# Performance work log

Measured on AMD Instinct MI355X. Metric: run time of the kernel, lower is better.

The kernel has to match this reference:

```python
import jax, jax.numpy as jnp
import numpy as np

B, T, C, H = 4, 2048, 1024, 16
INIT_STD = 0.02

def setup_inputs() -> dict:
    key = jax.random.key(0)
    ks = jax.random.split(key, 9)
    x = jax.random.normal(ks[0], (B, T, C), dtype=jnp.float32)
    def dense(kw):
        return jax.random.normal(kw, (C, C), dtype=jnp.float32) * INIT_STD
    return {
        "x": x,
        "Wq": dense(ks[1]), "bq": jnp.zeros((C,), jnp.float32),
        "Wk": dense(ks[2]), "bk": jnp.zeros((C,), jnp.float32),
        "Wv": dense(ks[3]), "bv": jnp.zeros((C,), jnp.float32),
        "Wo": dense(ks[4]), "bo": jnp.zeros((C,), jnp.float32),
    }

def reference(x, Wq, bq, Wk, bk, Wv, bv, Wo, bo):
    b, t, c = x.shape
    hd = c // H  # head dim
    # QKV projections, reshape to (B, H, T, hd)
    def split_heads(y):
        return jnp.transpose(y.reshape(b, t, H, hd), (0, 2, 1, 3))
    q = split_heads(x @ Wq + bq)
    k = split_heads(x @ Wk + bk)
    v = split_heads(x @ Wv + bv)
    scale = 1.0 / jnp.sqrt(jnp.float32(hd))
    att = jnp.einsum('bhqd,bhkd->bhqk', q, k) * scale  # [B,H,T,T]
    mask = jnp.tril(jnp.ones((t, t), dtype=bool))[None, None]
    att = jnp.where(mask, att, jnp.float32(-jnp.inf))
    att = jax.nn.softmax(att, axis=-1)
    y = jnp.einsum('bhqk,bhkd->bhqd', att, v)  # [B,H,T,hd]
    y = jnp.transpose(y, (0, 2, 1, 3)).reshape(b, t, c)
    return y @ Wo + bo
```

## Files before the change

kernel.cpp:

```cpp
#include <hip/hip_runtime.h>
#include <hip/hip_bf16.h>
#include <stdint.h>

typedef __bf16 bf16;
typedef __attribute__((ext_vector_type(8))) __bf16 bf16x8;
typedef __attribute__((ext_vector_type(4))) __bf16 bf16x4;
typedef __attribute__((ext_vector_type(4))) float f32x4;

constexpr int Bn = 4, Tn = 2048, Cn = 1024, Hn = 16, HD = 64;
constexpr int Mn = Bn * Tn;

__device__ __forceinline__ void gl_lds16(const void* g, void* l) {
  __builtin_amdgcn_global_load_lds(
      (const __attribute__((address_space(1))) void*)g,
      (__attribute__((address_space(3))) void*)l, 16u, 0, 0u);
}

__global__ __launch_bounds__(256) void k_cvt_x(const float* __restrict__ x,
                                               bf16* __restrict__ xb) {
  int i = (blockIdx.x * 256 + threadIdx.x) * 8;
  float4 a = *(const float4*)(x + i);
  float4 b = *(const float4*)(x + i + 4);
  bf16x8 v;
  v[0] = (bf16)a.x; v[1] = (bf16)a.y; v[2] = (bf16)a.z; v[3] = (bf16)a.w;
  v[4] = (bf16)b.x; v[5] = (bf16)b.y; v[6] = (bf16)b.z; v[7] = (bf16)b.w;
  *(bf16x8*)(xb + i) = v;
}

__global__ __launch_bounds__(256) void k_tw(const float* __restrict__ W0,
                                            const float* __restrict__ W1,
                                            const float* __restrict__ W2,
                                            const float* __restrict__ W3,
                                            bf16* __restrict__ WT) {
  __shared__ float tile[32][33];
  const float* W = (blockIdx.z == 0) ? W0 : (blockIdx.z == 1) ? W1
                  : (blockIdx.z == 2) ? W2 : W3;
  bf16* out = WT + (size_t)blockIdx.z * Cn * Cn;
  int tx = threadIdx.x & 31, ty = threadIdx.x >> 5;
  int gx = blockIdx.x * 32 + tx;
  int gy = blockIdx.y * 32;
#pragma unroll
  for (int j = 0; j < 32; j += 8)
    tile[ty + j][tx] = W[(size_t)(gy + ty + j) * Cn + gx];
  __syncthreads();
  int ox = blockIdx.y * 32 + tx;
  int oy = blockIdx.x * 32;
#pragma unroll
  for (int j = 0; j < 32; j += 8)
    out[(size_t)(oy + ty + j) * Cn + ox] = (bf16)tile[tx][ty + j];
}

__global__ __launch_bounds__(256) void k_gemm_qkv(const bf16* __restrict__ A,
                                                  const bf16* __restrict__ BT,
                                                  const float* __restrict__ bq,
                                                  const float* __restrict__ bk,
                                                  const float* __restrict__ bv,
                                                  bf16* __restrict__ out,
                                                  float qscale) {
  constexpr int KD = 1024;
  __shared__ __align__(16) bf16 As[128 * 64];
  __shared__ __align__(16) bf16 Bs[128 * 64];
  const int t = threadIdx.x;
  const int w = t >> 6, l = t & 63;
  const int b = blockIdx.x;
  const int k8 = b & 7, j = b >> 3;
  const int m0 = (j / 3) * 128, n0 = (3 * k8 + j % 3) * 128;
  const int wr = (w >> 1) * 64, wc = (w & 1) * 64;
  f32x4 acc[4][4] = {};

  for (int kt = 0; kt < KD; kt += 64) {
    __syncthreads();
#pragma unroll
    for (int i = 0; i < 4; ++i) {
      int c = i * 256 + t;
      int row = c >> 3;
      int seg = (c & 7) ^ (row & 7);
      gl_lds16(A + (size_t)(m0 + row) * KD + kt + seg * 8,
               (char*)As + i * 4096 + w * 1024);
      gl_lds16(BT + (size_t)(n0 + row) * KD + kt + seg * 8,
               (char*)Bs + i * 4096 + w * 1024);
    }
    __syncthreads();
#pragma unroll
    for (int kc = 0; kc < 2; ++kc) {
      bf16x8 af[4], bg[4];
#pragma unroll
      for (int mi = 0; mi < 4; ++mi) {
        int row = wr + mi * 16 + (l & 15);
        int off = (row * 128 + kc * 64 + (l >> 4) * 16) ^ ((row & 7) << 4);
        af[mi] = *(const bf16x8*)((const char*)As + off);
      }
#pragma unroll
      for (int ni = 0; ni < 4; ++ni) {
        int row = wc + ni * 16 + (l & 15);
        int off = (row * 128 + kc * 64 + (l >> 4) * 16) ^ ((row & 7) << 4);
        bg[ni] = *(const bf16x8*)((const char*)Bs + off);
      }
#pragma unroll
      for (int mi = 0; mi < 4; ++mi)
#pragma unroll
        for (int ni = 0; ni < 4; ++ni)
          acc[mi][ni] = __builtin_amdgcn_mfma_f32_16x16x32_bf16(
              af[mi], bg[ni], acc[mi][ni], 0, 0, 0);
    }
  }
  const int q16l = l & 15;
#pragma unroll
  for (int ni = 0; ni < 4; ++ni) {
    int colBase = n0 + wc + ni * 16;
    int which = colBase >> 10;
    const float* bp = (which == 0) ? bq : (which == 1) ? bk : bv;
    float scl = (which == 0) ? qscale : 1.0f;
    float bval = bp[(colBase & 1023) + q16l];
    int hh = (colBase >> 6) & 15;
    int dd = (colBase & 63) + q16l;
    size_t obase = (size_t)which * 8388608 + (size_t)hh * (Tn * HD) + dd;
#pragma unroll
    for (int mi = 0; mi < 4; ++mi) {
#pragma unroll
      for (int r = 0; r < 4; ++r) {
        int row = m0 + wr + mi * 16 + (l >> 4) * 4 + r;
        int bb = row >> 11, tt = row & 2047;
        float v = (acc[mi][ni][r] + bval) * scl;
        out[obase + ((size_t)bb * Hn * Tn + tt) * HD] = (bf16)v;
      }
    }
  }
}

__global__ __launch_bounds__(256) void k_gemm_o(const bf16* __restrict__ A,
                                                const bf16* __restrict__ BT,
                                                const float* __restrict__ bias,
                                                float* __restrict__ out) {
  constexpr int KD = 1024;
  __shared__ __align__(16) bf16 As[128 * 64];
  __shared__ __align__(16) bf16 Bs[128 * 64];
  const int t = threadIdx.x;
  const int w = t >> 6, l = t & 63;
  const int b = blockIdx.x;
  const int m0 = (b >> 3) * 128, n0 = (b & 7) * 128;
  const int wr = (w >> 1) * 64, wc = (w & 1) * 64;
  f32x4 acc[4][4] = {};

  for (int kt = 0; kt < KD; kt += 64) {
    __syncthreads();
#pragma unroll
    for (int i = 0; i < 4; ++i) {
      int c = i * 256 + t;
      int row = c >> 3;
      int seg = (c & 7) ^ (row & 7);
      gl_lds16(A + (size_t)(m0 + row) * KD + kt + seg * 8,
               (char*)As + i * 4096 + w * 1024);
      gl_lds16(BT + (size_t)(n0 + row) * KD + kt + seg * 8,
               (char*)Bs + i * 4096 + w * 1024);
    }
    __syncthreads();
#pragma unroll
    for (int kc = 0; kc < 2; ++kc) {
      bf16x8 af[4], bg[4];
#pragma unroll
      for (int mi = 0; mi < 4; ++mi) {
        int row = wr + mi * 16 + (l & 15);
        int off = (row * 128 + kc * 64 + (l >> 4) * 16) ^ ((row & 7) << 4);
        af[mi] = *(const bf16x8*)((const char*)As + off);
      }
#pragma unroll
      for (int ni = 0; ni < 4; ++ni) {
        int row = wc + ni * 16 + (l & 15);
        int off = (row * 128 + kc * 64 + (l >> 4) * 16) ^ ((row & 7) << 4);
        bg[ni] = *(const bf16x8*)((const char*)Bs + off);
      }
#pragma unroll
      for (int mi = 0; mi < 4; ++mi)
#pragma unroll
        for (int ni = 0; ni < 4; ++ni)
          acc[mi][ni] = __builtin_amdgcn_mfma_f32_16x16x32_bf16(
              af[mi], bg[ni], acc[mi][ni], 0, 0, 0);
    }
  }
#pragma unroll
  for (int ni = 0; ni < 4; ++ni) {
    int col = n0 + wc + ni * 16 + (l & 15);
    float bv = bias[col];
#pragma unroll
    for (int mi = 0; mi < 4; ++mi) {
#pragma unroll
      for (int r = 0; r < 4; ++r) {
        int row = m0 + wr + mi * 16 + (l >> 4) * 4 + r;
        out[(size_t)row * Cn + col] = acc[mi][ni][r] + bv;
      }
    }
  }
}

__global__ __launch_bounds__(512, 4) void k_attn(const bf16* __restrict__ Q,
                                                 const bf16* __restrict__ K,
                                                 const bf16* __restrict__ V,
                                                 bf16* __restrict__ Y) {
  __shared__ __align__(16) char smem[32768];
  const int t = threadIdx.x, w = t >> 6, l = t & 63;
  const int g = l >> 4, q16 = l & 15;
  const int wg = blockIdx.x;
  const int bh = wg & 63;
  const int qtile = 15 - (wg >> 6);
  const size_t base = (size_t)bh * Tn * HD;
  const bf16* Qh = Q + base;
  const bf16* Vh = V + base;
  const int qg = qtile * 128 + w * 16 + q16;

  bf16x8 aq[2];
#pragma unroll
  for (int kc = 0; kc < 2; ++kc)
    aq[kc] = *(const bf16x8*)(Qh + (size_t)qg * HD + kc * 32 + g * 8);

  const int xm = (q16 & 7) << 4;
  const int qkB0 = q16 * 128 + ((g * 16) ^ xm);
  const int qkB1 = q16 * 128 + ((64 + g * 16) ^ xm);
  const int innerL = (l >> 5) * 64 + ((l & 15) >> 2) * 16 +
                     (((l >> 4) & 1) * 4 + (l & 3)) * 2;
  int stb[8];
#pragma unroll
  for (int j = 0; j < 8; ++j)
    stb[j] = w * 1024 + j * 128 + (innerL ^ (j << 4));

  const int krow = w * 8 + (l >> 3);
  const int kseg = (l & 7) ^ (krow & 7);
  const bf16* kP = K + base + (size_t)krow * HD + kseg * 8;
  const bf16* vP = Vh + (size_t)l * HD + w * 8;

  f32x4 yacc[4] = {};
  float m_ = -1e30f, l_ = 0.f;
  const int nt = 2 * qtile + 2;
  const int it_mask = 2 * qtile + (w >= 4 ? 1 : 0);
  const int diag = (w & 3) * 16 + q16;

#define STAGE_K(KBUF)                           \
  {                                             \
    gl_lds16(kP, smem + (KBUF) + w * 1024);     \
    kP += 4096;                                 \
  }
#define WRITE_V(VBUF, a0)                               \
  {                                                     \
    _Pragma("unroll") for (int j = 0; j < 8; ++j)       \
      *(bf16*)(smem + (VBUF) + stb[j]) = a0[j];         \
  }
#define COMPUTE(KBUF, VBUF, DOMASK)                                          \
  {                                                                          \
    f32x4 s[4] = {};                                                         \
    __builtin_amdgcn_s_setprio(1);                                           \
    _Pragma("unroll") for (int nj = 0; nj < 4; ++nj) {                       \
      bf16x8 ak0 = *(const bf16x8*)(smem + (KBUF) + qkB0 + nj * 2048);       \
      s[nj] = __builtin_amdgcn_mfma_f32_16x16x32_bf16(ak0, aq[0], s[nj], 0, 0, 0); \
      bf16x8 ak1 = *(const bf16x8*)(smem + (KBUF) + qkB1 + nj * 2048);       \
      s[nj] = __builtin_amdgcn_mfma_f32_16x16x32_bf16(ak1, aq[1], s[nj], 0, 0, 0); \
    }                                                                        \
    __builtin_amdgcn_s_setprio(0);                                           \
    if (DOMASK) {                                                            \
      _Pragma("unroll") for (int nj = 0; nj < 4; ++nj)                       \
        _Pragma("unroll") for (int r = 0; r < 4; ++r)                        \
          if (nj * 16 + g * 4 + r > diag) s[nj][r] = -1e30f;                 \
    }                                                                        \
    float mx = fmaxf(fmaxf(fmaxf(s[0][0], s[0][1]), fmaxf(s[0][2], s[0][3])),\
                     fmaxf(fmaxf(s[1][0], s[1][1]), fmaxf(s[1][2], s[1][3])));\
    mx = fmaxf(mx, fmaxf(fmaxf(fmaxf(s[2][0], s[2][1]), fmaxf(s[2][2], s[2][3])),\
                         fmaxf(fmaxf(s[3][0], s[3][1]), fmaxf(s[3][2], s[3][3]))));\
    mx = fmaxf(mx, __shfl_xor(mx, 16));                                      \
    mx = fmaxf(mx, __shfl_xor(mx, 32));                                      \
    float mn = fmaxf(m_, mx);                                                \
    float fac = __builtin_amdgcn_exp2f(m_ - mn);                             \
    m_ = mn;                                                                 \
    float rs = 0.f;                                                          \
    _Pragma("unroll") for (int nj = 0; nj < 4; ++nj)                         \
      _Pragma("unroll") for (int r = 0; r < 4; ++r) {                        \
        float pv = __builtin_amdgcn_exp2f(s[nj][r] - mn);                    \
        s[nj][r] = pv;                                                       \
        rs += pv;                                                            \
      }                                                                      \
    rs += __shfl_xor(rs, 16);                                                \
    rs += __shfl_xor(rs, 32);                                                \
    l_ = l_ * fac + rs;                                                      \
    _Pragma("unroll") for (int ni = 0; ni < 4; ++ni)                         \
      _Pragma("unroll") for (int r = 0; r < 4; ++r) yacc[ni][r] *= fac;      \
    __builtin_amdgcn_s_setprio(1);                                           \
    _Pragma("unroll") for (int vkc = 0; vkc < 2; ++vkc) {                    \
      bf16x8 pb;                                                             \
      _Pragma("unroll") for (int j = 0; j < 4; ++j) {                        \
        pb[j] = (bf16)s[2 * vkc][j];                                         \
        pb[4 + j] = (bf16)s[2 * vkc + 1][j];                                 \
      }                                                                      \
      int vb = (vkc == 0) ? qkB0 : qkB1;                                     \
      _Pragma("unroll") for (int ni = 0; ni < 4; ++ni) {                     \
        bf16x8 va = *(const bf16x8*)(smem + (VBUF) + vb + ni * 2048);        \
        yacc[ni] = __builtin_amdgcn_mfma_f32_16x16x32_bf16(va, pb, yacc[ni], 0, 0, 0); \
      }                                                                      \
    }                                                                        \
    __builtin_amdgcn_s_setprio(0);                                           \
  }

  STAGE_K(0);
  {
    bf16x8 a0 = *(const bf16x8*)vP;
    vP += 4096;
    WRITE_V(16384, a0);
  }

  int it = 0;
  for (;;) {
    __syncthreads();
    bool more = (it + 1) < nt;
    bf16x8 a0;
    if (more) {
      STAGE_K(8192);
      a0 = *(const bf16x8*)vP;
      vP += 4096;
    }
    if (it <= it_mask) COMPUTE(0, 16384, it == it_mask);
    if (more) WRITE_V(24576, a0);
    if (++it >= nt) break;

    __syncthreads();
    more = (it + 1) < nt;
    if (more) {
      STAGE_K(0);
      a0 = *(const bf16x8*)vP;
      vP += 4096;
    }
    if (it <= it_mask) COMPUTE(8192, 24576, it == it_mask);
    if (more) WRITE_V(16384, a0);
    if (++it >= nt) break;
  }
#undef STAGE_K
#undef WRITE_V
#undef COMPUTE

  const int hh = bh & 15, bb = bh >> 4;
  float inv = 1.f / l_;
#pragma unroll
  for (int ni = 0; ni < 4; ++ni) {
    bf16x4 o;
#pragma unroll
    for (int r = 0; r < 4; ++r) o[r] = (bf16)(yacc[ni][r] * inv);
    int d0 = ni * 16 + g * 4;
    *(bf16x4*)&Y[(size_t)(bb * Tn + qg) * Cn + hh * HD + d0] = o;
  }
}

extern "C" void kernel_launch(void* const* d_in, const int* in_sizes, int n_in,
                              void* d_out, int out_size, void* d_ws,
                              size_t ws_size, hipStream_t stream) {
  const float* x  = (const float*)d_in[0];
  const float* Wq = (const float*)d_in[1];
  const float* bq = (const float*)d_in[2];
  const float* Wk = (const float*)d_in[3];
  const float* bk = (const float*)d_in[4];
  const float* Wv = (const float*)d_in[5];
  const float* bv = (const float*)d_in[6];
  const float* Wo = (const float*)d_in[7];
  const float* bo = (const float*)d_in[8];
  char* ws = (char*)d_ws;
  bf16* xb = (bf16*)ws;
  bf16* WT = (bf16*)(ws + (size_t)(16 << 20));
  bf16* Qh = (bf16*)(ws + (size_t)(24 << 20));
  bf16* Kh = (bf16*)(ws + (size_t)(40 << 20));
  bf16* Vh = (bf16*)(ws + (size_t)(56 << 20));
  float* out = (float*)d_out;

  const float QSCALE = 0.125f * 1.44269504088896f;

  k_cvt_x<<<4096, 256, 0, stream>>>(x, xb);
  k_tw<<<dim3(32, 32, 4), 256, 0, stream>>>(Wq, Wk, Wv, Wo, WT);
  k_gemm_qkv<<<1536, 256, 0, stream>>>(xb, WT, bq, bk, bv, Qh, QSCALE);
  k_attn<<<1024, 512, 0, stream>>>(Qh, Kh, Vh, xb);
  k_gemm_o<<<512, 256, 0, stream>>>(xb, WT + (3u << 20), bo, out);
}
```

Measured before the change: 161.4 us.

## Rewrite QKV GEMM with 256x256 tiles and double-buffered interleaved LDS prefetch

Replaces the 128x128 single-buffered QKV projection GEMM with a 512-thread kernel computing 256x256 tiles. LDS is double-buffered, and the next k-slice's global-to-LDS loads are issued in quarters between MFMA groups, using explicit vmcnt waits, raw barriers and priority hints. This raises operand reuse per loaded byte and hides global load latency behind MFMA work. In exchange it uses 128KB of LDS, which limits occupancy to one block per CU, and the 384-block grid fills the GPU unevenly.

```diff
diff --git a/kernel.cpp b/kernel.cpp
--- a/kernel.cpp
+++ b/kernel.cpp
@@ -50,79 +50,122 @@
     out[(size_t)(oy + ty + j) * Cn + ox] = (bf16)tile[tx][ty + j];
 }
 
-__global__ __launch_bounds__(256) void k_gemm_qkv(const bf16* __restrict__ A,
-                                                  const bf16* __restrict__ BT,
-                                                  const float* __restrict__ bq,
-                                                  const float* __restrict__ bk,
-                                                  const float* __restrict__ bv,
-                                                  bf16* __restrict__ out,
-                                                  float qscale) {
-  constexpr int KD = 1024;
-  __shared__ __align__(16) bf16 As[128 * 64];
-  __shared__ __align__(16) bf16 Bs[128 * 64];
-  const int t = threadIdx.x;
-  const int w = t >> 6, l = t & 63;
+__global__ __launch_bounds__(512, 2) void k_gemm_qkv8(
+    const bf16* __restrict__ A, const bf16* __restrict__ BT,
+    const float* __restrict__ bq, const float* __restrict__ bk,
+    const float* __restrict__ bv, bf16* __restrict__ out, float qscale) {
+  __shared__ __align__(16) char sm[131072];
+  const int t = threadIdx.x, w = t >> 6, l = t & 63;
+  const int g = l >> 4, q16 = l & 15;
+  const int wm = w >> 2, wn = w & 3;
   const int b = blockIdx.x;
-  const int k8 = b & 7, j = b >> 3;
-  const int m0 = (j / 3) * 128, n0 = (3 * k8 + j % 3) * 128;
-  const int wr = (w >> 1) * 64, wc = (w & 1) * 64;
-  f32x4 acc[4][4] = {};
-
-  for (int kt = 0; kt < KD; kt += 64) {
-    __syncthreads();
-#pragma unroll
-    for (int i = 0; i < 4; ++i) {
-      int c = i * 256 + t;
-      int row = c >> 3;
-      int seg = (c & 7) ^ (row & 7);
-      gl_lds16(A + (size_t)(m0 + row) * KD + kt + seg * 8,
-               (char*)As + i * 4096 + w * 1024);
-      gl_lds16(BT + (size_t)(n0 + row) * KD + kt + seg * 8,
-               (char*)Bs + i * 4096 + w * 1024);
-    }
-    __syncthreads();
-#pragma unroll
-    for (int kc = 0; kc < 2; ++kc) {
-      bf16x8 af[4], bg[4];
-#pragma unroll
-      for (int mi = 0; mi < 4; ++mi) {
-        int row = wr + mi * 16 + (l & 15);
-        int off = (row * 128 + kc * 64 + (l >> 4) * 16) ^ ((row & 7) << 4);
-        af[mi] = *(const bf16x8*)((const char*)As + off);
-      }
-#pragma unroll
-      for (int ni = 0; ni < 4; ++ni) {
-        int row = wc + ni * 16 + (l & 15);
-        int off = (row * 128 + kc * 64 + (l >> 4) * 16) ^ ((row & 7) << 4);
-        bg[ni] = *(const bf16x8*)((const char*)Bs + off);
-      }
-#pragma unroll
-      for (int mi = 0; mi < 4; ++mi)
-#pragma unroll
-        for (int ni = 0; ni < 4; ++ni)
-          acc[mi][ni] = __builtin_amdgcn_mfma_f32_16x16x32_bf16(
-              af[mi], bg[ni], acc[mi][ni], 0, 0, 0);
-    }
-  }
-  const int q16l = l & 15;
+  const int k8 = b & 7, idx = b >> 3;
+  const int n0 = ((k8 & 3) * 3 + idx % 3) * 256;
+  const int m0 = (idx / 3 + (k8 >> 2) * 16) * 256;
+
+  const int xm = (q16 & 7) << 4;
+  const int qkB0 = q16 * 128 + ((g * 16) ^ xm);
+  const int qkB1 = q16 * 128 + ((64 + g * 16) ^ xm);
+  const int aB = wm * 16384;
+  const int bB = 32768 + (wn >> 1) * 16384 + (wn & 1) * 8192;
+
+  const int row0 = t >> 3;
+  const int row1 = row0 + 64;
+  const int seg = (t & 7) ^ (row0 & 7);
+  const bf16* aS0 = A + (size_t)(m0 + row0) * 1024 + seg * 8;
+  const bf16* aS1 = A + (size_t)(m0 + row1) * 1024 + seg * 8;
+  const bf16* bS0 = BT + (size_t)(n0 + row0) * 1024 + seg * 8;
+  const bf16* bS1 = BT + (size_t)(n0 + row1) * 1024 + seg * 8;
+
+  f32x4 acc[8][4] = {};
+
+#define QSTG_A(NB, H, J)                                                  \
+  gl_lds16(aS0 + (H) * 131072 + (J) * 64, sm + (NB) + (H) * 16384 + w * 1024); \
+  gl_lds16(aS1 + (H) * 131072 + (J) * 64,                                 \
+           sm + (NB) + (H) * 16384 + 8192 + w * 1024);
+#define QSTG_B(NB, H, J)                                                  \
+  gl_lds16(bS0 + (H) * 131072 + (J) * 64,                                 \
+           sm + (NB) + 32768 + (H) * 16384 + w * 1024);                   \
+  gl_lds16(bS1 + (H) * 131072 + (J) * 64,                                 \
+           sm + (NB) + 32768 + (H) * 16384 + 8192 + w * 1024);
+#define QRD_A(DST, BANK, MI)                                              \
+  DST[0] = *(const bf16x8*)(sm + (BANK) + aB + (MI) * 2048 + qkB0);       \
+  DST[1] = *(const bf16x8*)(sm + (BANK) + aB + (MI) * 2048 + qkB1);
+#define QMFMA(AF, MI)                                                     \
+  _Pragma("unroll") for (int ni = 0; ni < 4; ++ni) {                      \
+    acc[MI][ni] = __builtin_amdgcn_mfma_f32_16x16x32_bf16(                \
+        AF[0], bfr[ni][0], acc[MI][ni], 0, 0, 0);                         \
+    acc[MI][ni] = __builtin_amdgcn_mfma_f32_16x16x32_bf16(                \
+        AF[1], bfr[ni][1], acc[MI][ni], 0, 0, 0);                         \
+  }
+
+  QSTG_A(0, 0, 0); QSTG_A(0, 1, 0); QSTG_B(0, 0, 0); QSTG_B(0, 1, 0);
+
+#pragma unroll
+  for (int j = 0; j < 16; ++j) {
+    const int BANK = (j & 1) ? 65536 : 0;
+    const int NB = (j & 1) ? 0 : 65536;
+    const bool more = j < 15;
+    if (more) { QSTG_A(NB, 0, j + 1); }
+    if (more) asm volatile("s_waitcnt vmcnt(2)" ::: "memory");
+    else      asm volatile("s_waitcnt vmcnt(0)" ::: "memory");
+    __builtin_amdgcn_sched_barrier(0);
+    __builtin_amdgcn_s_barrier();
+    __builtin_amdgcn_sched_barrier(0);
+    bf16x8 bfr[4][2];
+#pragma unroll
+    for (int ni = 0; ni < 4; ++ni) {
+      bfr[ni][0] = *(const bf16x8*)(sm + BANK + bB + ni * 2048 + qkB0);
+      bfr[ni][1] = *(const bf16x8*)(sm + BANK + bB + ni * 2048 + qkB1);
+    }
+    bf16x8 a0[2], a1[2], a2[2], a3[2];
+    QRD_A(a0, BANK, 0); QRD_A(a1, BANK, 1);
+    __builtin_amdgcn_s_setprio(1);
+    QMFMA(a0, 0); QMFMA(a1, 1);
+    __builtin_amdgcn_s_setprio(0);
+    __builtin_amdgcn_s_barrier();
+    if (more) { QSTG_A(NB, 1, j + 1); }
+    QRD_A(a2, BANK, 2); QRD_A(a3, BANK, 3);
+    __builtin_amdgcn_s_setprio(1);
+    QMFMA(a2, 2); QMFMA(a3, 3);
+    __builtin_amdgcn_s_setprio(0);
+    __builtin_amdgcn_s_barrier();
+    if (more) { QSTG_B(NB, 0, j + 1); }
+    QRD_A(a0, BANK, 4); QRD_A(a1, BANK, 5);
+    __builtin_amdgcn_s_setprio(1);
+    QMFMA(a0, 4); QMFMA(a1, 5);
+    __builtin_amdgcn_s_setprio(0);
+    __builtin_amdgcn_s_barrier();
+    if (more) { QSTG_B(NB, 1, j + 1); }
+    QRD_A(a2, BANK, 6); QRD_A(a3, BANK, 7);
+    __builtin_amdgcn_s_setprio(1);
+    QMFMA(a2, 6); QMFMA(a3, 7);
+    __builtin_amdgcn_s_setprio(0);
+    __builtin_amdgcn_s_barrier();
+  }
+#undef QSTG_A
+#undef QSTG_B
+#undef QRD_A
+#undef QMFMA
+
 #pragma unroll
   for (int ni = 0; ni < 4; ++ni) {
-    int colBase = n0 + wc + ni * 16;
+    int colBase = n0 + wn * 64 + ni * 16;
     int which = colBase >> 10;
     const float* bp = (which == 0) ? bq : (which == 1) ? bk : bv;
     float scl = (which == 0) ? qscale : 1.0f;
-    float bval = bp[(colBase & 1023) + q16l];
+    float bval = bp[(colBase & 1023) + q16];
     int hh = (colBase >> 6) & 15;
-    int dd = (colBase & 63) + q16l;
+    int dd = (colBase & 63) + q16;
     size_t obase = (size_t)which * 8388608 + (size_t)hh * (Tn * HD) + dd;
 #pragma unroll
-    for (int mi = 0; mi < 4; ++mi) {
+    for (int mi = 0; mi < 8; ++mi) {
 #pragma unroll
       for (int r = 0; r < 4; ++r) {
-        int row = m0 + wr + mi * 16 + (l >> 4) * 4 + r;
+        int row = m0 + wm * 128 + mi * 16 + g * 4 + r;
         int bb = row >> 11, tt = row & 2047;
-        float v = (acc[mi][ni][r] + bval) * scl;
-        out[obase + ((size_t)bb * Hn * Tn + tt) * HD] = (bf16)v;
+        out[obase + ((size_t)bb * Hn * Tn + tt) * HD] =
+            (bf16)((acc[mi][ni][r] + bval) * scl);
       }
     }
   }
@@ -369,7 +412,7 @@
 
   k_cvt_x<<<4096, 256, 0, stream>>>(x, xb);
   k_tw<<<dim3(32, 32, 4), 256, 0, stream>>>(Wq, Wk, Wv, Wo, WT);
-  k_gemm_qkv<<<1536, 256, 0, stream>>>(xb, WT, bq, bk, bv, Qh, QSCALE);
+  k_gemm_qkv8<<<384, 512, 0, stream>>>(xb, WT, bq, bk, bv, Qh, QSCALE);
   k_attn<<<1024, 512, 0, stream>>>(Qh, Kh, Vh, xb);
   k_gemm_o<<<512, 256, 0, stream>>>(xb, WT + (3u << 20), bo, out);
 }
```

Measured after the change: 158.3 us. About the same (-2.0%).

## Rewrite projection GEMMs with 8-wave double-buffered LDS pipeline and XCD-aware block mapping

Applied to the files above, without the earlier changes.

Both projection GEMMs (QKV and output) now share a macro-defined core that uses 512 threads (8 waves, 2x4 layout) per 128x128 tile. It double-buffers the 64-wide K slices in a 64 KB LDS area, prefetching the next slice with global_load_lds while MFMAs run on the current one. Waits use explicit vmcnt and s_barrier, and s_setprio is raised around the MFMA bursts. Block indices are remapped so consecutive blocks on the same XCD share tiles, which is meant to hide load latency and improve L2 reuse. The cost is higher LDS use per block (64 KB), which limits occupancy to about 2 blocks per CU, plus hand-tuned synchronization.

```diff
diff --git a/kernel.cpp b/kernel.cpp
--- a/kernel.cpp
+++ b/kernel.cpp
@@ -50,143 +50,132 @@
     out[(size_t)(oy + ty + j) * Cn + ox] = (bf16)tile[tx][ty + j];
 }
 
-__global__ __launch_bounds__(256) void k_gemm_qkv(const bf16* __restrict__ A,
-                                                  const bf16* __restrict__ BT,
-                                                  const float* __restrict__ bq,
-                                                  const float* __restrict__ bk,
-                                                  const float* __restrict__ bv,
-                                                  bf16* __restrict__ out,
-                                                  float qscale) {
-  constexpr int KD = 1024;
-  __shared__ __align__(16) bf16 As[128 * 64];
-  __shared__ __align__(16) bf16 Bs[128 * 64];
-  const int t = threadIdx.x;
-  const int w = t >> 6, l = t & 63;
-  const int b = blockIdx.x;
-  const int k8 = b & 7, j = b >> 3;
-  const int m0 = (j / 3) * 128, n0 = (3 * k8 + j % 3) * 128;
-  const int wr = (w >> 1) * 64, wc = (w & 1) * 64;
-  f32x4 acc[4][4] = {};
-
-  for (int kt = 0; kt < KD; kt += 64) {
-    __syncthreads();
-#pragma unroll
-    for (int i = 0; i < 4; ++i) {
-      int c = i * 256 + t;
-      int row = c >> 3;
-      int seg = (c & 7) ^ (row & 7);
-      gl_lds16(A + (size_t)(m0 + row) * KD + kt + seg * 8,
-               (char*)As + i * 4096 + w * 1024);
-      gl_lds16(BT + (size_t)(n0 + row) * KD + kt + seg * 8,
-               (char*)Bs + i * 4096 + w * 1024);
-    }
-    __syncthreads();
-#pragma unroll
-    for (int kc = 0; kc < 2; ++kc) {
-      bf16x8 af[4], bg[4];
-#pragma unroll
-      for (int mi = 0; mi < 4; ++mi) {
-        int row = wr + mi * 16 + (l & 15);
-        int off = (row * 128 + kc * 64 + (l >> 4) * 16) ^ ((row & 7) << 4);
-        af[mi] = *(const bf16x8*)((const char*)As + off);
-      }
-#pragma unroll
-      for (int ni = 0; ni < 4; ++ni) {
-        int row = wc + ni * 16 + (l & 15);
-        int off = (row * 128 + kc * 64 + (l >> 4) * 16) ^ ((row & 7) << 4);
-        bg[ni] = *(const bf16x8*)((const char*)Bs + off);
-      }
-#pragma unroll
-      for (int mi = 0; mi < 4; ++mi)
-#pragma unroll
-        for (int ni = 0; ni < 4; ++ni)
-          acc[mi][ni] = __builtin_amdgcn_mfma_f32_16x16x32_bf16(
-              af[mi], bg[ni], acc[mi][ni], 0, 0, 0);
-    }
-  }
-  const int q16l = l & 15;
-#pragma unroll
-  for (int ni = 0; ni < 4; ++ni) {
-    int colBase = n0 + wc + ni * 16;
+#define GEMM_CORE(ACC)                                                      \
+  const int t = threadIdx.x, l = t & 63, w = t >> 6;                        \
+  const int g = l >> 4, q16 = l & 15;                                       \
+  const int wm = w >> 2, wn = w & 3;                                        \
+  const int xm = (q16 & 7) << 4;                                            \
+  const int qkB0 = q16 * 128 + ((g * 16) ^ xm);                             \
+  const int qkB1 = q16 * 128 + ((64 + g * 16) ^ xm);                        \
+  const int srow = t >> 3;                                                  \
+  const int sseg = (t & 7) ^ (srow & 7);                                    \
+  const bf16* aP0 = A + (size_t)(m0 + srow) * 1024 + sseg * 8;              \
+  const bf16* aP1 = aP0 + 65536;                                            \
+  const bf16* bP0 = BT + (size_t)(n0 + srow) * 1024 + sseg * 8;             \
+  const bf16* bP1 = bP0 + 65536;                                            \
+  f32x4 ACC[4][2] = {};                                                     \
+                                            \
+  gl_lds16(aP0, sm + w * 1024);                                             \
+  gl_lds16(aP1, sm + 8192 + w * 1024);                                      \
+  gl_lds16(bP0, sm + 16384 + w * 1024);                                     \
+  gl_lds16(bP1, sm + 24576 + w * 1024);                                     \
+  _Pragma("unroll")                                                         \
+  for (int j = 0; j < 16; ++j) {                                            \
+    const int BK_ = (j & 1) ? 32768 : 0;                                    \
+    const int NB_ = 32768 - BK_;                                            \
+    const bool more = j < 15;                                               \
+    if (more) {                                                             \
+      gl_lds16(aP0 + (j + 1) * 64, sm + NB_ + w * 1024);                    \
+      gl_lds16(aP1 + (j + 1) * 64, sm + NB_ + 8192 + w * 1024);             \
+      gl_lds16(bP0 + (j + 1) * 64, sm + NB_ + 16384 + w * 1024);            \
+      gl_lds16(bP1 + (j + 1) * 64, sm + NB_ + 24576 + w * 1024);            \
+      asm volatile("s_waitcnt vmcnt(4)" ::: "memory");                      \
+    } else {                                                                \
+      asm volatile("s_waitcnt vmcnt(0)" ::: "memory");                      \
+    }                                                                       \
+    __builtin_amdgcn_sched_barrier(0);                                      \
+    __builtin_amdgcn_s_barrier();                                           \
+    bf16x8 bfr[2][2], af0[2], af1[2];                                       \
+    _Pragma("unroll") for (int ni = 0; ni < 2; ++ni) {                      \
+      bfr[ni][0] = *(const bf16x8*)(sm + BK_ + 16384 + wn * 4096 +          \
+                                    ni * 2048 + qkB0);                      \
+      bfr[ni][1] = *(const bf16x8*)(sm + BK_ + 16384 + wn * 4096 +          \
+                                    ni * 2048 + qkB1);                      \
+    }                                                                       \
+    af0[0] = *(const bf16x8*)(sm + BK_ + wm * 8192 + qkB0);                 \
+    af0[1] = *(const bf16x8*)(sm + BK_ + wm * 8192 + qkB1);                 \
+    af1[0] = *(const bf16x8*)(sm + BK_ + wm * 8192 + 2048 + qkB0);          \
+    af1[1] = *(const bf16x8*)(sm + BK_ + wm * 8192 + 2048 + qkB1);          \
+    __builtin_amdgcn_s_setprio(1);                                          \
+    _Pragma("unroll") for (int ni = 0; ni < 2; ++ni) {                      \
+      ACC[0][ni] = __builtin_amdgcn_mfma_f32_16x16x32_bf16(                 \
+          af0[0], bfr[ni][0], ACC[0][ni], 0, 0, 0);                         \
+      ACC[0][ni] = __builtin_amdgcn_mfma_f32_16x16x32_bf16(                 \
+          af0[1], bfr[ni][1], ACC[0][ni], 0, 0, 0);                         \
+      ACC[1][ni] = __builtin_amdgcn_mfma_f32_16x16x32_bf16(                 \
+          af1[0], bfr[ni][0], ACC[1][ni], 0, 0, 0);                         \
+      ACC[1][ni] = __builtin_amdgcn_mfma_f32_16x16x32_bf16(                 \
+          af1[1], bfr[ni][1], ACC[1][ni], 0, 0, 0);                         \
+    }                                                                       \
+    __builtin_amdgcn_s_setprio(0);                                          \
+    af0[0] = *(const bf16x8*)(sm + BK_ + wm * 8192 + 4096 + qkB0);          \
+    af0[1] = *(const bf16x8*)(sm + BK_ + wm * 8192 + 4096 + qkB1);          \
+    af1[0] = *(const bf16x8*)(sm + BK_ + wm * 8192 + 6144 + qkB0);          \
+    af1[1] = *(const bf16x8*)(sm + BK_ + wm * 8192 + 6144 + qkB1);          \
+    __builtin_amdgcn_s_setprio(1);                                          \
+    _Pragma("unroll") for (int ni = 0; ni < 2; ++ni) {                      \
+      ACC[2][ni] = __builtin_amdgcn_mfma_f32_16x16x32_bf16(                 \
+          af0[0], bfr[ni][0], ACC[2][ni], 0, 0, 0);                         \
+      ACC[2][ni] = __builtin_amdgcn_mfma_f32_16x16x32_bf16(                 \
+          af0[1], bfr[ni][1], ACC[2][ni], 0, 0, 0);                         \
+      ACC[3][ni] = __builtin_amdgcn_mfma_f32_16x16x32_bf16(                 \
+          af1[0], bfr[ni][0], ACC[3][ni], 0, 0, 0);                         \
+      ACC[3][ni] = __builtin_amdgcn_mfma_f32_16x16x32_bf16(                 \
+          af1[1], bfr[ni][1], ACC[3][ni], 0, 0, 0);                         \
+    }                                                                       \
+    __builtin_amdgcn_s_setprio(0);                                          \
+    __builtin_amdgcn_s_barrier();                                           \
+  }
+
+__global__ __launch_bounds__(512, 2) void k_gemm_qkv8(
+    const bf16* __restrict__ A, const bf16* __restrict__ BT,
+    const float* __restrict__ bq, const float* __restrict__ bk,
+    const float* __restrict__ bv, bf16* __restrict__ out, float qscale) {
+  __shared__ __align__(16) char sm[65536];
+  const int b0 = blockIdx.x;
+  const int blk = (b0 & 7) * 192 + (b0 >> 3);
+  const int m0 = (blk / 24) * 128, n0 = (blk % 24) * 128;
+  GEMM_CORE(acc)
+#pragma unroll
+  for (int ni = 0; ni < 2; ++ni) {
+    int colBase = n0 + wn * 32 + ni * 16;
     int which = colBase >> 10;
     const float* bp = (which == 0) ? bq : (which == 1) ? bk : bv;
     float scl = (which == 0) ? qscale : 1.0f;
-    float bval = bp[(colBase & 1023) + q16l];
+    float bval = bp[(colBase & 1023) + q16];
     int hh = (colBase >> 6) & 15;
-    int dd = (colBase & 63) + q16l;
+    int dd = (colBase & 63) + q16;
     size_t obase = (size_t)which * 8388608 + (size_t)hh * (Tn * HD) + dd;
 #pragma unroll
     for (int mi = 0; mi < 4; ++mi) {
 #pragma unroll
       for (int r = 0; r < 4; ++r) {
-        int row = m0 + wr + mi * 16 + (l >> 4) * 4 + r;
+        int row = m0 + wm * 64 + mi * 16 + g * 4 + r;
         int bb = row >> 11, tt = row & 2047;
-        float v = (acc[mi][ni][r] + bval) * scl;
-        out[obase + ((size_t)bb * Hn * Tn + tt) * HD] = (bf16)v;
+        out[obase + ((size_t)bb * Hn * Tn + tt) * HD] =
+            (bf16)((acc[mi][ni][r] + bval) * scl);
       }
     }
   }
 }
 
-__global__ __launch_bounds__(256) void k_gemm_o(const bf16* __restrict__ A,
-                                                const bf16* __restrict__ BT,
-                                                const float* __restrict__ bias,
-                                                float* __restrict__ out) {
-  constexpr int KD = 1024;
-  __shared__ __align__(16) bf16 As[128 * 64];
-  __shared__ __align__(16) bf16 Bs[128 * 64];
-  const int t = threadIdx.x;
-  const int w = t >> 6, l = t & 63;
-  const int b = blockIdx.x;
-  const int m0 = (b >> 3) * 128, n0 = (b & 7) * 128;
-  const int wr = (w >> 1) * 64, wc = (w & 1) * 64;
-  f32x4 acc[4][4] = {};
-
-  for (int kt = 0; kt < KD; kt += 64) {
-    __syncthreads();
-#pragma unroll
-    for (int i = 0; i < 4; ++i) {
-      int c = i * 256 + t;
-      int row = c >> 3;
-      int seg = (c & 7) ^ (row & 7);
-      gl_lds16(A + (size_t)(m0 + row) * KD + kt + seg * 8,
-               (char*)As + i * 4096 + w * 1024);
-      gl_lds16(BT + (size_t)(n0 + row) * KD + kt + seg * 8,
-               (char*)Bs + i * 4096 + w * 1024);
-    }
-    __syncthreads();
-#pragma unroll
-    for (int kc = 0; kc < 2; ++kc) {
-      bf16x8 af[4], bg[4];
-#pragma unroll
-      for (int mi = 0; mi < 4; ++mi) {
-        int row = wr + mi * 16 + (l & 15);
-        int off = (row * 128 + kc * 64 + (l >> 4) * 16) ^ ((row & 7) << 4);
-        af[mi] = *(const bf16x8*)((const char*)As + off);
-      }
-#pragma unroll
-      for (int ni = 0; ni < 4; ++ni) {
-        int row = wc + ni * 16 + (l & 15);
-        int off = (row * 128 + kc * 64 + (l >> 4) * 16) ^ ((row & 7) << 4);
-        bg[ni] = *(const bf16x8*)((const char*)Bs + off);
-      }
-#pragma unroll
-      for (int mi = 0; mi < 4; ++mi)
-#pragma unroll
-        for (int ni = 0; ni < 4; ++ni)
-          acc[mi][ni] = __builtin_amdgcn_mfma_f32_16x16x32_bf16(
-              af[mi], bg[ni], acc[mi][ni], 0, 0, 0);
-    }
-  }
-#pragma unroll
-  for (int ni = 0; ni < 4; ++ni) {
-    int col = n0 + wc + ni * 16 + (l & 15);
+__global__ __launch_bounds__(512, 2) void k_gemm_o8(
+    const bf16* __restrict__ A, const bf16* __restrict__ BT,
+    const float* __restrict__ bias, float* __restrict__ out) {
+  __shared__ __align__(16) char sm[65536];
+  const int b0 = blockIdx.x;
+  const int blk = (b0 & 7) * 64 + (b0 >> 3);
+  const int m0 = (blk >> 3) * 128, n0 = (blk & 7) * 128;
+  GEMM_CORE(acc)
+#pragma unroll
+  for (int ni = 0; ni < 2; ++ni) {
+    int col = n0 + wn * 32 + ni * 16 + q16;
     float bv = bias[col];
 #pragma unroll
     for (int mi = 0; mi < 4; ++mi) {
 #pragma unroll
       for (int r = 0; r < 4; ++r) {
-        int row = m0 + wr + mi * 16 + (l >> 4) * 4 + r;
+        int row = m0 + wm * 64 + mi * 16 + g * 4 + r;
         out[(size_t)row * Cn + col] = acc[mi][ni][r] + bv;
       }
     }
@@ -369,7 +358,7 @@
 
   k_cvt_x<<<4096, 256, 0, stream>>>(x, xb);
   k_tw<<<dim3(32, 32, 4), 256, 0, stream>>>(Wq, Wk, Wv, Wo, WT);
-  k_gemm_qkv<<<1536, 256, 0, stream>>>(xb, WT, bq, bk, bv, Qh, QSCALE);
+  k_gemm_qkv8<<<1536, 512, 0, stream>>>(xb, WT, bq, bk, bv, Qh, QSCALE);
   k_attn<<<1024, 512, 0, stream>>>(Qh, Kh, Vh, xb);
-  k_gemm_o<<<512, 256, 0, stream>>>(xb, WT + (3u << 20), bo, out);
-}
+  k_gemm_o8<<<512, 512, 0, stream>>>(xb, WT + (3u << 20), bo, out);
+}
```

Result: faster. 152.0 us (-5.9%).
